# Optimization experiments

Hardware: AMD Instinct MI355X
Metric: run time of the kernel (lower is better)

The kernel has to match this reference:

```python
import jax, jax.numpy as jnp
import numpy as np

N_NODES = 50000
N_EDGES = 1600000
N_GRAPHS = 512
IN_C, H1, H2, H3, OUT_C = 16, 64, 64, 128, 10


def setup_inputs() -> dict:
    key = jax.random.key(0)
    ks = jax.random.split(key, 12)
    x = jax.random.normal(ks[0], (N_NODES, IN_C), dtype=jnp.float32)
    edge_index = jax.random.randint(ks[1], (2, N_EDGES), 0, N_NODES, dtype=jnp.int64 if jax.config.jax_enable_x64 else jnp.int32)
    batch = jnp.sort(jax.random.randint(ks[2], (N_NODES,), 0, N_GRAPHS))
    s = 0.05
    return {
        "x": x,
        "edge_index": edge_index,
        "batch": batch,
        "W1": jax.random.normal(ks[3], (IN_C, H1), dtype=jnp.float32) * s,
        "b1": jnp.zeros((H1,), jnp.float32),
        "W2": jax.random.normal(ks[4], (H1, H2), dtype=jnp.float32) * s,
        "b2": jnp.zeros((H2,), jnp.float32),
        "Wf1": jax.random.normal(ks[5], (H2, H3), dtype=jnp.float32) * s,
        "bf1": jnp.zeros((H3,), jnp.float32),
        "Wf2": jax.random.normal(ks[6], (H3, OUT_C), dtype=jnp.float32) * s,
        "bf2": jnp.zeros((OUT_C,), jnp.float32),
    }


def reference(x, edge_index, batch, W1, b1, W2, b2, Wf1, bf1, Wf2, bf2):
    N = x.shape[0]
    self_idx = jnp.arange(N, dtype=edge_index.dtype)
    # PyG GCNConv default: add self-loops, symmetric normalization deg^-1/2
    src = jnp.concatenate([edge_index[0], self_idx])
    dst = jnp.concatenate([edge_index[1], self_idx])
    deg = jnp.zeros((N,), x.dtype).at[dst].add(1.0)  # >= 1 due to self-loops
    dinv = jax.lax.rsqrt(deg)
    norm = dinv[src] * dinv[dst]  # [E+N]

    def gcn_conv(h, W, b):
        hw = h @ W                                   # [N, C_out]
        msgs = hw[src] * norm[:, None]               # gather [E+N, C_out]
        return jax.ops.segment_sum(msgs, dst, num_segments=N) + b

    h = jax.nn.relu(gcn_conv(x, W1, b1))
    h = jax.nn.relu(gcn_conv(h, W2, b2))

    # global_mean_pool over graph ids
    counts = jax.ops.segment_sum(jnp.ones((N,), h.dtype), batch, num_segments=N_GRAPHS)
    sums = jax.ops.segment_sum(h, batch, num_segments=N_GRAPHS)
    pooled = sums / jnp.maximum(counts, 1.0)[:, None]  # [G, H2]

    out = pooled @ Wf1 + bf1
    out = out @ Wf2 + bf2
    return out
```

## Files before the change

### kernel.cpp

```cpp
#include <hip/hip_runtime.h>

#define N_NODES   50000
#define N_EDGES   1600000
#define N_GRAPHS  512
#define IN_C      16
#define H1        64
#define H2        64
#define H3        128
#define OUT_C     10

#define NBKT      196
#define CHUNK     4096
#define CAP       12288

typedef unsigned int  uint;
typedef unsigned short ushort;


__global__ void __launch_bounds__(256) k_binB(const int* __restrict__ src,
                                              const int* __restrict__ dst,
                                              int* __restrict__ bkt_fill,
                                              uint* __restrict__ bucket_edges) {
    __shared__ int  lcnt[NBKT];
    __shared__ int  loff[NBKT];
    __shared__ int  gbase[NBKT];
    __shared__ int  tmp[256];
    __shared__ uint stage[CHUNK];
    int tid = threadIdx.x;
    long long e0 = (long long)blockIdx.x * CHUNK;
    int cn = (int)((N_EDGES - e0) < CHUNK ? (N_EDGES - e0) : CHUNK);

    for (int i = tid; i < NBKT; i += 256) lcnt[i] = 0;
    __syncthreads();

    uint pk[16]; int rk[16]; int bkr[16];
#pragma unroll
    for (int k = 0; k < 16; ++k) {
        int i = k * 256 + tid;
        pk[k] = 0; rk[k] = -1; bkr[k] = 0;
        if (i < cn) {
            int e = (int)e0 + i;
            uint d = (uint)dst[e], s = (uint)src[e];
            pk[k] = (d << 16) | s;
            bkr[k] = (int)(d >> 8);
            rk[k] = atomicAdd(&lcnt[bkr[k]], 1);
        }
    }
    __syncthreads();

    int v = (tid < NBKT) ? lcnt[tid] : 0;
    tmp[tid] = v;
    __syncthreads();
    for (int s = 1; s < 256; s <<= 1) {
        int t = (tid >= s) ? tmp[tid - s] : 0;
        __syncthreads();
        tmp[tid] += t;
        __syncthreads();
    }
    if (tid < NBKT) loff[tid] = tmp[tid] - v;
    if (tid < NBKT && v > 0) gbase[tid] = atomicAdd(&bkt_fill[tid], v);
    __syncthreads();

#pragma unroll
    for (int k = 0; k < 16; ++k)
        if (rk[k] >= 0) stage[loff[bkr[k]] + rk[k]] = pk[k];
    __syncthreads();

    for (int i = tid; i < cn; i += 256) {
        uint p = stage[i];
        int b = (int)(p >> 24);
        int pos = gbase[b] + (i - loff[b]);
        if (pos < CAP) bucket_edges[(size_t)b * CAP + pos] = p;
    }
}


__global__ void __launch_bounds__(256) k_bkt_csr(const int* __restrict__ bkt_fill,
                                                 const uint* __restrict__ bucket_edges,
                                                 const float* __restrict__ x,
                                                 int* __restrict__ rowbeg,
                                                 int* __restrict__ rowend,
                                                 float* __restrict__ dinv,
                                                 float* __restrict__ xs,
                                                 ushort* __restrict__ src_sorted) {
    __shared__ int ncnt[256];
    __shared__ int noff[256];
    __shared__ int tmp[256];
    __shared__ ushort su[CAP];
    int b = blockIdx.x, tid = threadIdx.x;
    int base = b * CAP;
    int cntE = bkt_fill[b];
    if (cntE > CAP) cntE = CAP;

    ncnt[tid] = 0;
    __syncthreads();
    for (int i = tid; i < cntE; i += 256) {
        uint p = bucket_edges[base + i];
        atomicAdd(&ncnt[(p >> 16) & 255], 1);
    }
    __syncthreads();

    int v = ncnt[tid];
    tmp[tid] = v;
    __syncthreads();
    for (int s = 1; s < 256; s <<= 1) {
        int t = (tid >= s) ? tmp[tid - s] : 0;
        __syncthreads();
        tmp[tid] += t;
        __syncthreads();
    }
    noff[tid] = tmp[tid] - v;

    int n = b * 256 + tid;
    if (n < N_NODES) {
        rowbeg[n] = base + (tmp[tid] - v);
        rowend[n] = base + tmp[tid];
        float dv = rsqrtf((float)(v + 1));
        dinv[n] = dv;
        const float4* xr = (const float4*)(x + (size_t)n * IN_C);
        float4* xo = (float4*)(xs + (size_t)n * IN_C);
#pragma unroll
        for (int j = 0; j < 4; ++j) {
            float4 t = xr[j];
            t.x *= dv; t.y *= dv; t.z *= dv; t.w *= dv;
            xo[j] = t;
        }
    }

    ncnt[tid] = 0;
    __syncthreads();
    for (int i = tid; i < cntE; i += 256) {
        uint p = bucket_edges[base + i];
        int l = (p >> 16) & 255;
        int r = atomicAdd(&ncnt[l], 1);
        int pos = noff[l] + r;
        if (pos < CAP) su[pos] = (ushort)(p & 0xFFFF);
    }
    __syncthreads();
    for (int i = tid; i < cntE; i += 256)
        src_sorted[base + i] = su[i];
}


__global__ void __launch_bounds__(256) k_agg16(
    const int* __restrict__ rowbeg, const int* __restrict__ rowend,
    const ushort* __restrict__ src_sorted,
    const float* __restrict__ dinv, const float* __restrict__ tab,
    float* __restrict__ out)
{
    int n = (int)(blockIdx.x * 4 + (threadIdx.x >> 6));
    if (n >= N_NODES) return;
    int lane = threadIdx.x & 63;
    int slot = lane >> 2;
    int c4 = (lane & 3) << 2;

    int beg = rowbeg[n], end = rowend[n];
    float4 acc = {0.f,0.f,0.f,0.f}, acc2 = {0.f,0.f,0.f,0.f};

    if (slot == 0)
        acc = *(const float4*)(tab + (size_t)n * 16 + c4);

    for (int i = beg; i < end; i += 32) {
        int i0 = i + slot, i1 = i0 + 16;
        bool k0 = i0 < end, k1 = i1 < end;
        int s0 = k0 ? (int)src_sorted[i0] : 0;
        int s1 = k1 ? (int)src_sorted[i1] : 0;
        float m0 = k0 ? 1.f : 0.f;
        float m1 = k1 ? 1.f : 0.f;
        float4 h0 = *(const float4*)(tab + (size_t)s0 * 16 + c4);
        float4 h1 = *(const float4*)(tab + (size_t)s1 * 16 + c4);
        acc.x  = fmaf(h0.x, m0, acc.x);   acc.y  = fmaf(h0.y, m0, acc.y);
        acc.z  = fmaf(h0.z, m0, acc.z);   acc.w  = fmaf(h0.w, m0, acc.w);
        acc2.x = fmaf(h1.x, m1, acc2.x);  acc2.y = fmaf(h1.y, m1, acc2.y);
        acc2.z = fmaf(h1.z, m1, acc2.z);  acc2.w = fmaf(h1.w, m1, acc2.w);
    }
    acc.x += acc2.x; acc.y += acc2.y; acc.z += acc2.z; acc.w += acc2.w;

#pragma unroll
    for (int off = 4; off <= 32; off <<= 1) {
        acc.x += __shfl_xor(acc.x, off);
        acc.y += __shfl_xor(acc.y, off);
        acc.z += __shfl_xor(acc.z, off);
        acc.w += __shfl_xor(acc.w, off);
    }
    if (slot == 0) {
        float di = dinv[n];
        acc.x *= di; acc.y *= di; acc.z *= di; acc.w *= di;
        *(float4*)(out + (size_t)n * 16 + c4) = acc;
    }
}


__global__ void __launch_bounds__(256) k_agg64(
    const int* __restrict__ rowbeg, const int* __restrict__ rowend,
    const ushort* __restrict__ src_sorted,
    const float* __restrict__ dinv, const float* __restrict__ u,
    const float* __restrict__ b2, float* __restrict__ h2)
{
    int n = (int)(blockIdx.x * 4 + (threadIdx.x >> 6));
    if (n >= N_NODES) return;
    int lane = threadIdx.x & 63;
    int slot = lane >> 4;
    int c4 = (lane & 15) << 2;

    int beg = rowbeg[n], end = rowend[n];
    float4 acc = {0.f,0.f,0.f,0.f}, acc2 = {0.f,0.f,0.f,0.f};

    if (slot == 0)
        acc = *(const float4*)(u + (size_t)n * 64 + c4);

    for (int i = beg; i < end; i += 8) {
        int i0 = i + slot, i1 = i0 + 4;
        bool k0 = i0 < end, k1 = i1 < end;
        int s0 = k0 ? (int)src_sorted[i0] : 0;
        int s1 = k1 ? (int)src_sorted[i1] : 0;
        float m0 = k0 ? 1.f : 0.f;
        float m1 = k1 ? 1.f : 0.f;
        float4 h0 = *(const float4*)(u + (size_t)s0 * 64 + c4);
        float4 h1 = *(const float4*)(u + (size_t)s1 * 64 + c4);
        acc.x  = fmaf(h0.x, m0, acc.x);   acc.y  = fmaf(h0.y, m0, acc.y);
        acc.z  = fmaf(h0.z, m0, acc.z);   acc.w  = fmaf(h0.w, m0, acc.w);
        acc2.x = fmaf(h1.x, m1, acc2.x);  acc2.y = fmaf(h1.y, m1, acc2.y);
        acc2.z = fmaf(h1.z, m1, acc2.z);  acc2.w = fmaf(h1.w, m1, acc2.w);
    }
    acc.x += acc2.x; acc.y += acc2.y; acc.z += acc2.z; acc.w += acc2.w;

    acc.x += __shfl_xor(acc.x, 16);  acc.y += __shfl_xor(acc.y, 16);
    acc.z += __shfl_xor(acc.z, 16);  acc.w += __shfl_xor(acc.w, 16);
    acc.x += __shfl_xor(acc.x, 32);  acc.y += __shfl_xor(acc.y, 32);
    acc.z += __shfl_xor(acc.z, 32);  acc.w += __shfl_xor(acc.w, 32);

    if (slot == 0) {
        float di = dinv[n];
        float4 bv = *(const float4*)(b2 + c4);
        float4 o = {fmaf(acc.x, di, bv.x), fmaf(acc.y, di, bv.y),
                    fmaf(acc.z, di, bv.z), fmaf(acc.w, di, bv.w)};
        *(float4*)(h2 + (size_t)n * 64 + c4) = o;
    }
}


__global__ void __launch_bounds__(256) k_gemm1(const float* __restrict__ in,
                                               const float* __restrict__ W,
                                               const float* __restrict__ bias,
                                               const float* __restrict__ dinv,
                                               float* __restrict__ out) {
    __shared__ float Wl[IN_C * 64];
    int tid = threadIdx.x;
    for (int i = tid; i < IN_C * 16; i += 256)
        ((float4*)Wl)[i] = ((const float4*)W)[i];
    __syncthreads();

    int n = blockIdx.x * 32 + (tid >> 3);
    int c0 = (tid & 7) * 8;
    if (n >= N_NODES) return;

    const float4* row = (const float4*)(in + (size_t)n * IN_C);
    float acc[8];
#pragma unroll
    for (int j = 0; j < 8; ++j) acc[j] = 0.f;
#pragma unroll
    for (int kb = 0; kb < IN_C / 4; ++kb) {
        float4 r = row[kb];
        const float* wr = &Wl[(kb * 4) * 64 + c0];
        float rk[4] = {r.x, r.y, r.z, r.w};
#pragma unroll
        for (int k = 0; k < 4; ++k) {
            float4 w0 = *(const float4*)(wr + k * 64);
            float4 w1 = *(const float4*)(wr + k * 64 + 4);
            acc[0] += rk[k] * w0.x;  acc[1] += rk[k] * w0.y;
            acc[2] += rk[k] * w0.z;  acc[3] += rk[k] * w0.w;
            acc[4] += rk[k] * w1.x;  acc[5] += rk[k] * w1.y;
            acc[6] += rk[k] * w1.z;  acc[7] += rk[k] * w1.w;
        }
    }
    float di = dinv[n];
    float4 bv0 = *(const float4*)(bias + c0);
    float4 bv1 = *(const float4*)(bias + c0 + 4);
    float4 o0 = {fmaxf(acc[0] + bv0.x, 0.f) * di, fmaxf(acc[1] + bv0.y, 0.f) * di,
                 fmaxf(acc[2] + bv0.z, 0.f) * di, fmaxf(acc[3] + bv0.w, 0.f) * di};
    float4 o1 = {fmaxf(acc[4] + bv1.x, 0.f) * di, fmaxf(acc[5] + bv1.y, 0.f) * di,
                 fmaxf(acc[6] + bv1.z, 0.f) * di, fmaxf(acc[7] + bv1.w, 0.f) * di};
    *(float4*)(out + (size_t)n * 64 + c0)     = o0;
    *(float4*)(out + (size_t)n * 64 + c0 + 4) = o1;
}


__global__ void __launch_bounds__(256) k_gemm2(const float* __restrict__ in,
                                               const float* __restrict__ W,
                                               float* __restrict__ out) {
    __shared__ float Wl[H1 * 64];
    int tid = threadIdx.x;
#pragma unroll
    for (int i = tid; i < H1 * 16; i += 256)
        ((float4*)Wl)[i] = ((const float4*)W)[i];
    __syncthreads();

    int n = blockIdx.x * 32 + (tid >> 3);
    int c0 = (tid & 7) * 8;
    if (n >= N_NODES) return;

    float acc[8];
#pragma unroll
    for (int j = 0; j < 8; ++j) acc[j] = 0.f;

#pragma unroll 4
    for (int kb = 0; kb < H1 / 4; ++kb) {
        float4 r = *(const float4*)(in + (size_t)n * 64 + kb * 4);
        const float* wr = &Wl[(kb * 4) * 64 + c0];
        float rk[4] = {r.x, r.y, r.z, r.w};
#pragma unroll
        for (int k = 0; k < 4; ++k) {
            float4 w0 = *(const float4*)(wr + k * 64);
            float4 w1 = *(const float4*)(wr + k * 64 + 4);
            acc[0] += rk[k] * w0.x;  acc[1] += rk[k] * w0.y;
            acc[2] += rk[k] * w0.z;  acc[3] += rk[k] * w0.w;
            acc[4] += rk[k] * w1.x;  acc[5] += rk[k] * w1.y;
            acc[6] += rk[k] * w1.z;  acc[7] += rk[k] * w1.w;
        }
    }
    *(float4*)(out + (size_t)n * 64 + c0)     = (float4){acc[0], acc[1], acc[2], acc[3]};
    *(float4*)(out + (size_t)n * 64 + c0 + 4) = (float4){acc[4], acc[5], acc[6], acc[7]};
}


__global__ void __launch_bounds__(256) k_pool2(const int* __restrict__ batch,
                                               const float* __restrict__ h,
                                               float* __restrict__ pool,
                                               float* __restrict__ gcnt) {
    int wave = (blockIdx.x * blockDim.x + threadIdx.x) >> 6;
    int lane = threadIdx.x & 63;
    int n0 = wave * 64;
    if (n0 >= N_NODES) return;
    int nend = n0 + 64 < N_NODES ? n0 + 64 : N_NODES;
    int g = batch[n0];
    float acc = 0.f, c = 0.f;
    for (int n = n0; n < nend; ++n) {
        int gn = batch[n];
        if (gn != g) {
            atomicAdd(&pool[g * 64 + lane], acc);
            if (lane == 0) atomicAdd(&gcnt[g], c);
            acc = 0.f; c = 0.f; g = gn;
        }
        acc += fmaxf(h[(size_t)n * 64 + lane], 0.f);
        c += 1.f;
    }
    atomicAdd(&pool[g * 64 + lane], acc);
    if (lane == 0) atomicAdd(&gcnt[g], c);
}


__global__ void __launch_bounds__(128)
k_mlp(const float* __restrict__ pool, const float* __restrict__ cnt,
      const float* __restrict__ Wf1, const float* __restrict__ bf1,
      const float* __restrict__ Wf2, const float* __restrict__ bf2,
      float* __restrict__ out) {
    int g = blockIdx.x;
    int tid = threadIdx.x;
    __shared__ float p[H2];
    __shared__ float tbuf[H3];
    float inv = 1.0f / fmaxf(cnt[g], 1.0f);
    if (tid < H2) p[tid] = pool[g * H2 + tid] * inv;
    __syncthreads();
    {
        float acc = bf1[tid];
#pragma unroll
        for (int k = 0; k < H2; ++k) acc += p[k] * Wf1[k * H3 + tid];
        tbuf[tid] = acc;
    }
    __syncthreads();
    if (tid < OUT_C) {
        float acc = bf2[tid];
#pragma unroll
        for (int m = 0; m < H3; ++m) acc += tbuf[m] * Wf2[m * OUT_C + tid];
        out[g * OUT_C + tid] = acc;
    }
}


extern "C" void kernel_launch(void* const* d_in, const int* in_sizes, int n_in,
                              void* d_out, int out_size, void* d_ws, size_t ws_size,
                              hipStream_t stream) {
    const float* x    = (const float*)d_in[0];
    const int*   ei   = (const int*)  d_in[1];
    const int*   batch= (const int*)  d_in[2];
    const float* W1   = (const float*)d_in[3];
    const float* b1   = (const float*)d_in[4];
    const float* W2   = (const float*)d_in[5];
    const float* b2   = (const float*)d_in[6];
    const float* Wf1  = (const float*)d_in[7];
    const float* bf1  = (const float*)d_in[8];
    const float* Wf2  = (const float*)d_in[9];
    const float* bf2  = (const float*)d_in[10];
    float* out = (float*)d_out;

    const int* src = ei;
    const int* dst = ei + N_EDGES;

    char* ws = (char*)d_ws;
    size_t off = 0;
    auto alloc = [&](size_t bytes) {
        char* p = ws + off;
        off += (bytes + 255) & ~size_t(255);
        return p;
    };
    int*    bkt_fill   = (int*)   alloc(NBKT * sizeof(int));
    float*  pool       = (float*) alloc(N_GRAPHS * H2 * sizeof(float));
    float*  gcnt       = (float*) alloc(N_GRAPHS * sizeof(float));
    size_t  zero_bytes = off;
    float*  dinv       = (float*) alloc(N_NODES * sizeof(float));
    int*    rowbeg     = (int*)   alloc(N_NODES * sizeof(int));
    int*    rowend     = (int*)   alloc(N_NODES * sizeof(int));
    ushort* src_sorted = (ushort*)alloc((size_t)NBKT * CAP * sizeof(ushort));
    float*  xs         = (float*) alloc((size_t)N_NODES * IN_C * sizeof(float));
    float*  ax         = (float*) alloc((size_t)N_NODES * IN_C * sizeof(float));
    float*  bufA       = (float*) alloc((size_t)N_NODES * 64 * sizeof(float));
    float*  bufB       = (float*) alloc((size_t)N_NODES * 64 * sizeof(float));
    uint*   bucket_edges = (uint*)bufB;
    (void)ws_size;

    const int BLK = 256;
    int gE  = (N_EDGES + CHUNK - 1) / CHUNK;
    int gG  = (N_NODES + 31) / 32;
    int gA  = (N_NODES + 3) / 4;
    int gPW = ((N_NODES + 63) / 64 * 64 + BLK - 1) / BLK;

    hipMemsetAsync(bkt_fill, 0, zero_bytes, stream);

    k_binB   <<<gE, BLK, 0, stream>>>(src, dst, bkt_fill, bucket_edges);
    k_bkt_csr<<<NBKT, BLK, 0, stream>>>(bkt_fill, bucket_edges, x,
                                        rowbeg, rowend, dinv, xs, src_sorted);

    k_agg16<<<gA, BLK, 0, stream>>>(rowbeg, rowend, src_sorted, dinv, xs, ax);
    k_gemm1<<<gG, BLK, 0, stream>>>(ax, W1, b1, dinv, bufA);

    k_gemm2<<<gG, BLK, 0, stream>>>(bufA, W2, bufB);
    k_agg64<<<gA, BLK, 0, stream>>>(rowbeg, rowend, src_sorted, dinv, bufB, b2, bufA);

    k_pool2<<<gPW, BLK, 0, stream>>>(batch, bufA, pool, gcnt);
    k_mlp  <<<N_GRAPHS, 128, 0, stream>>>(pool, gcnt, Wf1, bf1, Wf2, bf2, out);
}
```

Baseline: 163.6 us.

## Fuse layer GEMMs and store aggregation features as bf16

Merges the two per-node GEMM kernels into one, keeping the intermediate hidden layer in shared memory rather than round-tripping it through global memory. The second-layer features are stored as packed bf16, which halves the bytes read by the 64-channel gather aggregation. That aggregation is restructured so each lane handles 8 channels and each wave covers 8 edges per step with 4-way unrolling, giving more loads in flight. The cost is reduced precision of the gathered messages (bf16 rounding) and higher shared memory use per block.

```diff
diff --git a/kernel.cpp b/kernel.cpp
--- a/kernel.cpp
+++ b/kernel.cpp
@@ -191,136 +191,164 @@
 }
 
 
-__global__ void __launch_bounds__(256) k_agg64(
+__device__ __forceinline__ uint f2bf(float f) {
+    uint b = __float_as_uint(f);
+    return (b + 0x7fffu + ((b >> 16) & 1u)) >> 16;
+}
+
+__global__ void __launch_bounds__(256) k_gemm12(const float* __restrict__ ax,
+                                                const float* __restrict__ W1,
+                                                const float* __restrict__ b1,
+                                                const float* __restrict__ W2,
+                                                const float* __restrict__ dinv,
+                                                uint* __restrict__ ubf) {
+    __shared__ float W1l[IN_C * 64];
+    __shared__ float W2l[H1 * 64];
+    __shared__ float tl[32 * 64];
+    int tid = threadIdx.x;
+
+    ((float4*)W1l)[tid] = ((const float4*)W1)[tid];
+#pragma unroll
+    for (int i = tid; i < H1 * 16; i += 256)
+        ((float4*)W2l)[i] = ((const float4*)W2)[i];
+    __syncthreads();
+
+    int ln = tid >> 3;
+    int n = blockIdx.x * 32 + ln;
+    int c0 = (tid & 7) * 8;
+    bool valid = n < N_NODES;
+
+    float acc[8];
+#pragma unroll
+    for (int j = 0; j < 8; ++j) acc[j] = 0.f;
+    if (valid) {
+        const float4* row = (const float4*)(ax + (size_t)n * IN_C);
+#pragma unroll
+        for (int kb = 0; kb < IN_C / 4; ++kb) {
+            float4 r = row[kb];
+            const float* wr = &W1l[(kb * 4) * 64 + c0];
+            float rk[4] = {r.x, r.y, r.z, r.w};
+#pragma unroll
+            for (int k = 0; k < 4; ++k) {
+                float4 w0 = *(const float4*)(wr + k * 64);
+                float4 w1 = *(const float4*)(wr + k * 64 + 4);
+                acc[0] += rk[k] * w0.x;  acc[1] += rk[k] * w0.y;
+                acc[2] += rk[k] * w0.z;  acc[3] += rk[k] * w0.w;
+                acc[4] += rk[k] * w1.x;  acc[5] += rk[k] * w1.y;
+                acc[6] += rk[k] * w1.z;  acc[7] += rk[k] * w1.w;
+            }
+        }
+    }
+    float di = valid ? dinv[n] : 0.f;
+    float4 bv0 = *(const float4*)(b1 + c0);
+    float4 bv1 = *(const float4*)(b1 + c0 + 4);
+    float* tr = &tl[ln * 64 + c0];
+    tr[0] = fmaxf(acc[0] + bv0.x, 0.f) * di;
+    tr[1] = fmaxf(acc[1] + bv0.y, 0.f) * di;
+    tr[2] = fmaxf(acc[2] + bv0.z, 0.f) * di;
+    tr[3] = fmaxf(acc[3] + bv0.w, 0.f) * di;
+    tr[4] = fmaxf(acc[4] + bv1.x, 0.f) * di;
+    tr[5] = fmaxf(acc[5] + bv1.y, 0.f) * di;
+    tr[6] = fmaxf(acc[6] + bv1.z, 0.f) * di;
+    tr[7] = fmaxf(acc[7] + bv1.w, 0.f) * di;
+    __syncthreads();
+
+    float u[8];
+#pragma unroll
+    for (int j = 0; j < 8; ++j) u[j] = 0.f;
+    const float* tn = &tl[ln * 64];
+#pragma unroll 4
+    for (int kb = 0; kb < H1 / 4; ++kb) {
+        float4 r = *(const float4*)(tn + kb * 4);
+        const float* wr = &W2l[(kb * 4) * 64 + c0];
+        float rk[4] = {r.x, r.y, r.z, r.w};
+#pragma unroll
+        for (int k = 0; k < 4; ++k) {
+            float4 w0 = *(const float4*)(wr + k * 64);
+            float4 w1 = *(const float4*)(wr + k * 64 + 4);
+            u[0] += rk[k] * w0.x;  u[1] += rk[k] * w0.y;
+            u[2] += rk[k] * w0.z;  u[3] += rk[k] * w0.w;
+            u[4] += rk[k] * w1.x;  u[5] += rk[k] * w1.y;
+            u[6] += rk[k] * w1.z;  u[7] += rk[k] * w1.w;
+        }
+    }
+    if (valid) {
+        uint4 pk;
+        pk.x = f2bf(u[0]) | (f2bf(u[1]) << 16);
+        pk.y = f2bf(u[2]) | (f2bf(u[3]) << 16);
+        pk.z = f2bf(u[4]) | (f2bf(u[5]) << 16);
+        pk.w = f2bf(u[6]) | (f2bf(u[7]) << 16);
+        ((uint4*)ubf)[(size_t)n * 8 + (tid & 7)] = pk;
+    }
+}
+
+
+__global__ void __launch_bounds__(256) k_agg64bf(
     const int* __restrict__ rowbeg, const int* __restrict__ rowend,
     const ushort* __restrict__ src_sorted,
-    const float* __restrict__ dinv, const float* __restrict__ u,
+    const float* __restrict__ dinv, const uint* __restrict__ ubf,
     const float* __restrict__ b2, float* __restrict__ h2)
 {
     int n = (int)(blockIdx.x * 4 + (threadIdx.x >> 6));
     if (n >= N_NODES) return;
     int lane = threadIdx.x & 63;
-    int slot = lane >> 4;
-    int c4 = (lane & 15) << 2;
+    int slot = lane >> 3;
+    int l8 = lane & 7;
+    const uint4* U = (const uint4*)ubf;
 
     int beg = rowbeg[n], end = rowend[n];
-    float4 acc = {0.f,0.f,0.f,0.f}, acc2 = {0.f,0.f,0.f,0.f};
-
-    if (slot == 0)
-        acc = *(const float4*)(u + (size_t)n * 64 + c4);
-
-    for (int i = beg; i < end; i += 8) {
-        int i0 = i + slot, i1 = i0 + 4;
-        bool k0 = i0 < end, k1 = i1 < end;
-        int s0 = k0 ? (int)src_sorted[i0] : 0;
-        int s1 = k1 ? (int)src_sorted[i1] : 0;
-        float m0 = k0 ? 1.f : 0.f;
-        float m1 = k1 ? 1.f : 0.f;
-        float4 h0 = *(const float4*)(u + (size_t)s0 * 64 + c4);
-        float4 h1 = *(const float4*)(u + (size_t)s1 * 64 + c4);
-        acc.x  = fmaf(h0.x, m0, acc.x);   acc.y  = fmaf(h0.y, m0, acc.y);
-        acc.z  = fmaf(h0.z, m0, acc.z);   acc.w  = fmaf(h0.w, m0, acc.w);
-        acc2.x = fmaf(h1.x, m1, acc2.x);  acc2.y = fmaf(h1.y, m1, acc2.y);
-        acc2.z = fmaf(h1.z, m1, acc2.z);  acc2.w = fmaf(h1.w, m1, acc2.w);
-    }
-    acc.x += acc2.x; acc.y += acc2.y; acc.z += acc2.z; acc.w += acc2.w;
-
-    acc.x += __shfl_xor(acc.x, 16);  acc.y += __shfl_xor(acc.y, 16);
-    acc.z += __shfl_xor(acc.z, 16);  acc.w += __shfl_xor(acc.w, 16);
-    acc.x += __shfl_xor(acc.x, 32);  acc.y += __shfl_xor(acc.y, 32);
-    acc.z += __shfl_xor(acc.z, 32);  acc.w += __shfl_xor(acc.w, 32);
+    float acc[8];
+#pragma unroll
+    for (int j = 0; j < 8; ++j) acc[j] = 0.f;
+
+    if (slot == 0) {
+        uint4 v = U[(size_t)n * 8 + l8];
+        uint d[4] = {v.x, v.y, v.z, v.w};
+#pragma unroll
+        for (int k = 0; k < 4; ++k) {
+            acc[2*k]   = __uint_as_float(d[k] << 16);
+            acc[2*k+1] = __uint_as_float(d[k] & 0xFFFF0000u);
+        }
+    }
+
+    for (int i = beg; i < end; i += 32) {
+#pragma unroll
+        for (int k = 0; k < 4; ++k) {
+            int idx = i + slot + 8 * k;
+            bool kk = idx < end;
+            int s = kk ? (int)src_sorted[idx] : 0;
+            float m = kk ? 1.f : 0.f;
+            uint4 v = U[(size_t)s * 8 + l8];
+            acc[0] = fmaf(__uint_as_float(v.x << 16),         m, acc[0]);
+            acc[1] = fmaf(__uint_as_float(v.x & 0xFFFF0000u), m, acc[1]);
+            acc[2] = fmaf(__uint_as_float(v.y << 16),         m, acc[2]);
+            acc[3] = fmaf(__uint_as_float(v.y & 0xFFFF0000u), m, acc[3]);
+            acc[4] = fmaf(__uint_as_float(v.z << 16),         m, acc[4]);
+            acc[5] = fmaf(__uint_as_float(v.z & 0xFFFF0000u), m, acc[5]);
+            acc[6] = fmaf(__uint_as_float(v.w << 16),         m, acc[6]);
+            acc[7] = fmaf(__uint_as_float(v.w & 0xFFFF0000u), m, acc[7]);
+        }
+    }
+
+#pragma unroll
+    for (int off = 8; off <= 32; off <<= 1) {
+#pragma unroll
+        for (int j = 0; j < 8; ++j)
+            acc[j] += __shfl_xor(acc[j], off);
+    }
 
     if (slot == 0) {
         float di = dinv[n];
-        float4 bv = *(const float4*)(b2 + c4);
-        float4 o = {fmaf(acc.x, di, bv.x), fmaf(acc.y, di, bv.y),
-                    fmaf(acc.z, di, bv.z), fmaf(acc.w, di, bv.w)};
-        *(float4*)(h2 + (size_t)n * 64 + c4) = o;
-    }
-}
-
-
-__global__ void __launch_bounds__(256) k_gemm1(const float* __restrict__ in,
-                                               const float* __restrict__ W,
-                                               const float* __restrict__ bias,
-                                               const float* __restrict__ dinv,
-                                               float* __restrict__ out) {
-    __shared__ float Wl[IN_C * 64];
-    int tid = threadIdx.x;
-    for (int i = tid; i < IN_C * 16; i += 256)
-        ((float4*)Wl)[i] = ((const float4*)W)[i];
-    __syncthreads();
-
-    int n = blockIdx.x * 32 + (tid >> 3);
-    int c0 = (tid & 7) * 8;
-    if (n >= N_NODES) return;
-
-    const float4* row = (const float4*)(in + (size_t)n * IN_C);
-    float acc[8];
-#pragma unroll
-    for (int j = 0; j < 8; ++j) acc[j] = 0.f;
-#pragma unroll
-    for (int kb = 0; kb < IN_C / 4; ++kb) {
-        float4 r = row[kb];
-        const float* wr = &Wl[(kb * 4) * 64 + c0];
-        float rk[4] = {r.x, r.y, r.z, r.w};
-#pragma unroll
-        for (int k = 0; k < 4; ++k) {
-            float4 w0 = *(const float4*)(wr + k * 64);
-            float4 w1 = *(const float4*)(wr + k * 64 + 4);
-            acc[0] += rk[k] * w0.x;  acc[1] += rk[k] * w0.y;
-            acc[2] += rk[k] * w0.z;  acc[3] += rk[k] * w0.w;
-            acc[4] += rk[k] * w1.x;  acc[5] += rk[k] * w1.y;
-            acc[6] += rk[k] * w1.z;  acc[7] += rk[k] * w1.w;
-        }
-    }
-    float di = dinv[n];
-    float4 bv0 = *(const float4*)(bias + c0);
-    float4 bv1 = *(const float4*)(bias + c0 + 4);
-    float4 o0 = {fmaxf(acc[0] + bv0.x, 0.f) * di, fmaxf(acc[1] + bv0.y, 0.f) * di,
-                 fmaxf(acc[2] + bv0.z, 0.f) * di, fmaxf(acc[3] + bv0.w, 0.f) * di};
-    float4 o1 = {fmaxf(acc[4] + bv1.x, 0.f) * di, fmaxf(acc[5] + bv1.y, 0.f) * di,
-                 fmaxf(acc[6] + bv1.z, 0.f) * di, fmaxf(acc[7] + bv1.w, 0.f) * di};
-    *(float4*)(out + (size_t)n * 64 + c0)     = o0;
-    *(float4*)(out + (size_t)n * 64 + c0 + 4) = o1;
-}
-
-
-__global__ void __launch_bounds__(256) k_gemm2(const float* __restrict__ in,
-                                               const float* __restrict__ W,
-                                               float* __restrict__ out) {
-    __shared__ float Wl[H1 * 64];
-    int tid = threadIdx.x;
-#pragma unroll
-    for (int i = tid; i < H1 * 16; i += 256)
-        ((float4*)Wl)[i] = ((const float4*)W)[i];
-    __syncthreads();
-
-    int n = blockIdx.x * 32 + (tid >> 3);
-    int c0 = (tid & 7) * 8;
-    if (n >= N_NODES) return;
-
-    float acc[8];
-#pragma unroll
-    for (int j = 0; j < 8; ++j) acc[j] = 0.f;
-
-#pragma unroll 4
-    for (int kb = 0; kb < H1 / 4; ++kb) {
-        float4 r = *(const float4*)(in + (size_t)n * 64 + kb * 4);
-        const float* wr = &Wl[(kb * 4) * 64 + c0];
-        float rk[4] = {r.x, r.y, r.z, r.w};
-#pragma unroll
-        for (int k = 0; k < 4; ++k) {
-            float4 w0 = *(const float4*)(wr + k * 64);
-            float4 w1 = *(const float4*)(wr + k * 64 + 4);
-            acc[0] += rk[k] * w0.x;  acc[1] += rk[k] * w0.y;
-            acc[2] += rk[k] * w0.z;  acc[3] += rk[k] * w0.w;
-            acc[4] += rk[k] * w1.x;  acc[5] += rk[k] * w1.y;
-            acc[6] += rk[k] * w1.z;  acc[7] += rk[k] * w1.w;
-        }
-    }
-    *(float4*)(out + (size_t)n * 64 + c0)     = (float4){acc[0], acc[1], acc[2], acc[3]};
-    *(float4*)(out + (size_t)n * 64 + c0 + 4) = (float4){acc[4], acc[5], acc[6], acc[7]};
+        int c8 = l8 * 8;
+        float4 bv0 = *(const float4*)(b2 + c8);
+        float4 bv1 = *(const float4*)(b2 + c8 + 4);
+        float4 o0 = {fmaf(acc[0], di, bv0.x), fmaf(acc[1], di, bv0.y),
+                     fmaf(acc[2], di, bv0.z), fmaf(acc[3], di, bv0.w)};
+        float4 o1 = {fmaf(acc[4], di, bv1.x), fmaf(acc[5], di, bv1.y),
+                     fmaf(acc[6], di, bv1.z), fmaf(acc[7], di, bv1.w)};
+        *(float4*)(h2 + (size_t)n * 64 + c8)     = o0;
+        *(float4*)(h2 + (size_t)n * 64 + c8 + 4) = o1;
+    }
 }
 
 
@@ -417,6 +445,7 @@
     float*  bufA       = (float*) alloc((size_t)N_NODES * 64 * sizeof(float));
     float*  bufB       = (float*) alloc((size_t)N_NODES * 64 * sizeof(float));
     uint*   bucket_edges = (uint*)bufB;
+    uint*   ubf          = (uint*)bufB;
     (void)ws_size;
 
     const int BLK = 256;
@@ -432,10 +461,10 @@
                                         rowbeg, rowend, dinv, xs, src_sorted);
 
     k_agg16<<<gA, BLK, 0, stream>>>(rowbeg, rowend, src_sorted, dinv, xs, ax);
-    k_gemm1<<<gG, BLK, 0, stream>>>(ax, W1, b1, dinv, bufA);
-
-    k_gemm2<<<gG, BLK, 0, stream>>>(bufA, W2, bufB);
-    k_agg64<<<gA, BLK, 0, stream>>>(rowbeg, rowend, src_sorted, dinv, bufB, b2, bufA);
+
+    k_gemm12<<<gG, BLK, 0, stream>>>(ax, W1, b1, W2, dinv, ubf);
+
+    k_agg64bf<<<gA, BLK, 0, stream>>>(rowbeg, rowend, src_sorted, dinv, ubf, b2, bufA);
 
     k_pool2<<<gPW, BLK, 0, stream>>>(batch, bufA, pool, gcnt);
     k_mlp  <<<N_GRAPHS, 128, 0, stream>>>(pool, gcnt, Wf1, bf1, Wf2, bf2, out);
```

Result: faster. 142.0 us (-13.2%).
